# Optimization experiments

Hardware: AMD Instinct MI355X
Metric: run time of the kernel (lower is better)

The kernel has to match this reference:

```python
import jax, jax.numpy as jnp
import numpy as np

B, IN, OUT, GD, TD, H, W, L = 16, 512, 256, 256, 256, 32, 32, 32
EPS_BN = 1e-5


def _conv2d(x, w, pad):
    return jax.lax.conv_general_dilated(
        x, w, window_strides=(1, 1), padding=[(pad, pad), (pad, pad)],
        dimension_numbers=("NCHW", "OIHW", "NCHW"))


def _up2(x):
    return jnp.repeat(jnp.repeat(x, 2, axis=2), 2, axis=3)


def _l2n(v):  # F.normalize(p=2, dim=1), eps=1e-12
    n = jnp.sqrt(jnp.sum(v * v, axis=1, keepdims=True))
    return v / jnp.maximum(n, 1e-12)


def _context(img_embs, words_embs, mask):
    i = _l2n(img_embs)            # [B, TD, P]
    wd = _l2n(words_embs)         # [B, TD, L]
    sim = jnp.einsum("bcp,bcl->bpl", i, wd)
    sim = jnp.where(mask[:, None, :], -jnp.inf, sim)
    attn = jax.nn.softmax(sim, axis=-1)
    return jnp.einsum("bpl,bcl->bcp", attn, wd)  # [B, TD, P]


def _bn(x, w, b):  # training-mode BatchNorm2d, biased variance
    m = jnp.mean(x, axis=(0, 2, 3), keepdims=True)
    v = jnp.var(x, axis=(0, 2, 3), keepdims=True)
    return (x - m) * jax.lax.rsqrt(v + EPS_BN) * w[None, :, None, None] + b[None, :, None, None]


def setup_inputs():
    key = jax.random.key(0)
    ks = jax.random.split(key, 16)
    s = 0.02
    COND = GD + TD
    return {
        "x": jax.random.normal(ks[0], (B, IN, H, W), jnp.float32),
        "global_cond": jax.random.normal(ks[1], (B, GD), jnp.float32),
        "words_embs": jax.random.normal(ks[2], (B, TD, L), jnp.float32),
        "mask": jax.random.randint(ks[3], (B, L), 0, 2).astype(bool),
        "w_img1": jax.random.normal(ks[4], (TD, IN), jnp.float32) * s,
        "w_img2": jax.random.normal(ks[5], (TD, OUT), jnp.float32) * s,
        "w_c1": jax.random.normal(ks[6], (OUT, IN, 3, 3), jnp.float32) * s,
        "w_c2": jax.random.normal(ks[7], (OUT, OUT, 3, 3), jnp.float32) * s,
        "bn1_w": jnp.ones((IN,), jnp.float32),
        "bn1_b": jnp.zeros((IN,), jnp.float32),
        "bn2_w": jnp.ones((OUT,), jnp.float32),
        "bn2_b": jnp.zeros((OUT,), jnp.float32),
        "w_g1": jax.random.normal(ks[8], (IN, COND), jnp.float32) * s,
        "b_g1": jnp.zeros((IN,), jnp.float32),
        "w_b1": jax.random.normal(ks[9], (IN, COND), jnp.float32) * s,
        "b_b1": jnp.zeros((IN,), jnp.float32),
        "w_g2": jax.random.normal(ks[10], (OUT, COND), jnp.float32) * s,
        "b_g2": jnp.zeros((OUT,), jnp.float32),
        "w_b2": jax.random.normal(ks[11], (OUT, COND), jnp.float32) * s,
        "b_b2": jnp.zeros((OUT,), jnp.float32),
        "w_sc": jax.random.normal(ks[12], (OUT, IN, 1, 1), jnp.float32) * s,
        "b_sc": jnp.zeros((OUT,), jnp.float32),
    }


def reference(x, global_cond, words_embs, mask,
              w_img1, w_img2, w_c1, w_c2,
              bn1_w, bn1_b, bn2_w, bn2_b,
              w_g1, b_g1, w_b1, b_b1,
              w_g2, b_g2, w_b2, b_b2,
              w_sc, b_sc):
    # ---- residual path, stage 1 ----
    img1 = jnp.einsum("tc,bcp->btp", w_img1, x.reshape(B, IN, H * W))
    ctx1 = _context(img1, words_embs, mask)                 # [B, TD, H*W]
    gc = jnp.broadcast_to(global_cond[:, :, None], (B, GD, H * W))
    cond1 = jnp.concatenate([gc, ctx1], axis=1)             # [B, GD+TD, H*W]
    gamma1 = jnp.einsum("oc,bcp->bop", w_g1, cond1) + b_g1[None, :, None]
    beta1 = jnp.einsum("oc,bcp->bop", w_b1, cond1) + b_b1[None, :, None]
    out = gamma1.reshape(B, IN, H, W) * _bn(x, bn1_w, bn1_b) + beta1.reshape(B, IN, H, W)
    out = jax.nn.relu(out)
    out = _up2(out)                                         # [B, IN, 2H, 2W]
    out = _conv2d(out, w_c1, 1)                             # [B, OUT, 2H, 2W]
    h2, w2 = 2 * H, 2 * W
    # ---- residual path, stage 2 ----
    img2 = jnp.einsum("tc,bcp->btp", w_img2, out.reshape(B, OUT, h2 * w2))
    ctx2 = _context(img2, words_embs, mask)                 # [B, TD, h2*w2]
    gc2 = jnp.broadcast_to(global_cond[:, :, None], (B, GD, h2 * w2))
    cond2 = jnp.concatenate([gc2, ctx2], axis=1)
    gamma2 = jnp.einsum("oc,bcp->bop", w_g2, cond2) + b_g2[None, :, None]
    beta2 = jnp.einsum("oc,bcp->bop", w_b2, cond2) + b_b2[None, :, None]
    out = gamma2.reshape(B, OUT, h2, w2) * _bn(out, bn2_w, bn2_b) + beta2.reshape(B, OUT, h2, w2)
    out = jax.nn.relu(out)
    out = _conv2d(out, w_c2, 1)
    # ---- shortcut ----
    sc = _conv2d(_up2(x), w_sc, 0) + b_sc[None, :, None, None]
    return out + sc
```

## Files before the change

kernel.cpp:

```cpp
#include <hip/hip_runtime.h>
#include <hip/hip_bf16.h>
#include <math.h>

#define NB 16
#define CIN1 512
#define COUT 256
#define GD 256
#define TD 256
#define LL 32
#define P1 1024
#define P2 4096
#define CONDC 512

typedef __attribute__((ext_vector_type(8))) short bf16x8;
typedef __attribute__((ext_vector_type(4))) float f32x4;
typedef unsigned short u16;

__device__ __forceinline__ u16 f2b(float f) {
  __hip_bfloat16 h = __float2bfloat16(f);
  return *(u16*)&h;
}
__device__ __forceinline__ float b2f(u16 v) {
  unsigned u = ((unsigned)v) << 16;
  float f;
  __builtin_memcpy(&f, &u, 4);
  return f;
}

template <bool BF>
__global__ void bn_stats_kernel(const void* xv, float* __restrict__ mean,
                                float* __restrict__ rstd, int C, int HW) {
  int c = blockIdx.x, t = threadIdx.x;
  float s = 0.f, sq = 0.f;
  for (int b = 0; b < NB; ++b) {
    size_t base = ((size_t)b * C + c) * HW;
    for (int i = t; i < HW; i += 256) {
      float v = BF ? b2f(((const u16*)xv)[base + i]) : ((const float*)xv)[base + i];
      s += v; sq += v * v;
    }
  }
  __shared__ float ss[256], sq2[256];
  ss[t] = s; sq2[t] = sq; __syncthreads();
  for (int o = 128; o > 0; o >>= 1) {
    if (t < o) { ss[t] += ss[t + o]; sq2[t] += sq2[t + o]; }
    __syncthreads();
  }
  if (t == 0) {
    float n = (float)NB * (float)HW;
    float m = ss[0] / n;
    float v = sq2[0] / n - m * m;
    mean[c] = m;
    rstd[c] = rsqrtf(v + 1e-5f);
  }
}

__global__ void wdn_kernel(const float* __restrict__ we, float* __restrict__ wdn) {
  int b = blockIdx.x >> 5, l = blockIdx.x & 31;
  int t = threadIdx.x;
  const float* base = we + (size_t)b * TD * LL + l;
  float v[4]; float sq = 0.f;
#pragma unroll
  for (int k = 0; k < 4; ++k) { v[k] = base[(size_t)(t * 4 + k) * LL]; sq += v[k] * v[k]; }
#pragma unroll
  for (int o = 32; o > 0; o >>= 1) sq += __shfl_xor(sq, o);
  float r = 1.f / fmaxf(sqrtf(sq), 1e-12f);
  float* ob = wdn + (size_t)b * TD * LL + l;
#pragma unroll
  for (int k = 0; k < 4; ++k) ob[(size_t)(t * 4 + k) * LL] = v[k] * r;
}

__global__ void gvec_kernel(const float* __restrict__ Wg, const float* __restrict__ bias,
                            const float* __restrict__ gc, float* __restrict__ outv, int O) {
  int o = blockIdx.x * 64 + threadIdx.x;
  int b = blockIdx.y;
  if (o >= O) return;
  const float* wr = Wg + (size_t)o * CONDC;
  const float* g = gc + (size_t)b * GD;
  float s = 0.f;
  for (int c = 0; c < GD; ++c) s += wr[c] * g[c];
  outv[(size_t)b * O + o] = s + bias[o];
}

__global__ __launch_bounds__(256) void attnctx_kernel(
    const u16* __restrict__ img, const float* __restrict__ wdn,
    const int* __restrict__ mask, u16* __restrict__ ctx, int P) {
  __shared__ u16 imgT[64 * 72];
  __shared__ u16 wdnT[32 * 264];
  __shared__ u16 wdnC[256 * 40];
  __shared__ u16 attnB[64 * 40];
  __shared__ float sqP[4][64];
  __shared__ float rnL[64];
  const int b = blockIdx.y, p0 = blockIdx.x * 64;
  const int tid = threadIdx.x;
  const int w = tid >> 6, lane = tid & 63;
  const int l15 = lane & 15, lg = lane >> 4;
  const u16* ib = img + (size_t)b * TD * P;
  const float* wb = wdn + (size_t)b * TD * LL;

  for (int i = tid; i < TD * LL; i += 256) {
    int t = i >> 5, l = i & 31;
    u16 v = f2b(wb[i]);
    wdnT[l * 264 + t] = v;
    wdnC[t * 40 + l] = v;
  }

  f32x4 s0 = {}, s1 = {};
  float ssq = 0.f;
  for (int q = 0; q < 4; ++q) {
#pragma unroll
    for (int i = 0; i < 16; i += 2) {
      int t = q * 64 + w * 16 + i;
      u16 h0 = ib[(size_t)t * P + p0 + lane];
      u16 h1 = ib[(size_t)(t + 1) * P + p0 + lane];
      float v0 = b2f(h0), v1 = b2f(h1);
      ssq += v0 * v0 + v1 * v1;
      unsigned pk = (unsigned)h0 | ((unsigned)h1 << 16);
      *(unsigned*)(imgT + lane * 72 + w * 16 + i) = pk;
    }
    __syncthreads();
#pragma unroll
    for (int ks = 0; ks < 2; ++ks) {
      bf16x8 a = *(const bf16x8*)(imgT + (w * 16 + l15) * 72 + ks * 32 + lg * 8);
      bf16x8 b0 = *(const bf16x8*)(wdnT + l15 * 264 + q * 64 + ks * 32 + lg * 8);
      bf16x8 b1 = *(const bf16x8*)(wdnT + (16 + l15) * 264 + q * 64 + ks * 32 + lg * 8);
      s0 = __builtin_amdgcn_mfma_f32_16x16x32_bf16(a, b0, s0, 0, 0, 0);
      s1 = __builtin_amdgcn_mfma_f32_16x16x32_bf16(a, b1, s1, 0, 0, 0);
    }
    __syncthreads();
  }
  sqP[w][lane] = ssq;
  __syncthreads();
  if (tid < 64) {
    float s = sqP[0][tid] + sqP[1][tid] + sqP[2][tid] + sqP[3][tid];
    rnL[tid] = 1.f / fmaxf(sqrtf(s), 1e-12f);
  }
  __syncthreads();
  const bool m0 = mask[b * LL + l15] != 0;
  const bool m1 = mask[b * LL + 16 + l15] != 0;
#pragma unroll
  for (int k = 0; k < 4; ++k) {
    float rn = rnL[w * 16 + lg * 4 + k];
    float v0 = m0 ? -INFINITY : s0[k] * rn;
    float v1 = m1 ? -INFINITY : s1[k] * rn;
    float mx = fmaxf(v0, v1);
#pragma unroll
    for (int o = 1; o < 16; o <<= 1) mx = fmaxf(mx, __shfl_xor(mx, o));
    float e0 = expf(v0 - mx), e1 = expf(v1 - mx);
    float sm = e0 + e1;
#pragma unroll
    for (int o = 1; o < 16; o <<= 1) sm += __shfl_xor(sm, o);
    float inv = 1.f / sm;
    int px = w * 16 + lg * 4 + k;
    attnB[px * 40 + l15] = f2b(e0 * inv);
    attnB[px * 40 + 16 + l15] = f2b(e1 * inv);
  }
  __syncthreads();
  f32x4 acc[4][4] = {};
  bf16x8 bfr[4];
#pragma unroll
  for (int pt = 0; pt < 4; ++pt)
    bfr[pt] = *(const bf16x8*)(attnB + (pt * 16 + l15) * 40 + lg * 8);
#pragma unroll
  for (int cc = 0; cc < 4; ++cc) {
    bf16x8 a = *(const bf16x8*)(wdnC + ((w * 4 + cc) * 16 + l15) * 40 + lg * 8);
#pragma unroll
    for (int pt = 0; pt < 4; ++pt)
      acc[cc][pt] = __builtin_amdgcn_mfma_f32_16x16x32_bf16(a, bfr[pt], acc[cc][pt], 0, 0, 0);
  }
#pragma unroll
  for (int cc = 0; cc < 4; ++cc) {
#pragma unroll
    for (int pt = 0; pt < 4; ++pt) {
#pragma unroll
      for (int k = 0; k < 4; ++k) {
        int c = (w * 4 + cc) * 16 + lg * 4 + k;
        ctx[((size_t)b * TD + c) * P + p0 + pt * 16 + l15] = f2b(acc[cc][pt][k]);
      }
    }
  }
}

template <bool XB, bool YB>
__global__ __launch_bounds__(256, 2) void gemm_mfma_kernel(
    const float* __restrict__ W, int ldw, int c_off,
    const void* __restrict__ Xv, const float* __restrict__ vec,
    void* __restrict__ Yv, int T, int C, int P) {
  __shared__ u16 Wl[2][128 * 44];
  __shared__ u16 Xl[2][128 * 40];
  const int b = blockIdx.z;
  const int t0 = blockIdx.y * 128, p0 = blockIdx.x * 128;
  const int tid = threadIdx.x;
  const int w = tid >> 6, lane = tid & 63;
  const int wo = w >> 1, wq = w & 1;
  const int l15 = lane & 15, lg = lane >> 4;
  const int wr = tid >> 1, wcH = tid & 1;
  const int xr = tid >> 3, xcG = tid & 7;
  const int csw = xr ^ ((xcG & 3) << 3);
  const float* wsrc = W + (size_t)(t0 + wr) * ldw + c_off + wcH * 16;
  const float* xsrc32 = XB ? nullptr : (const float*)Xv + (size_t)b * C * P + (size_t)xr * P + p0 + xcG * 16;
  const u16* xsrc16 = XB ? (const u16*)Xv + (size_t)b * C * P + (size_t)xr * P + p0 + xcG * 16 : nullptr;
  const int NK = C / 32;
  f32x4 acc[4][4] = {};
  float4 wreg[4];
  u16 xst[16];

#pragma unroll
  for (int j = 0; j < 4; ++j) wreg[j] = *(const float4*)(wsrc + j * 4);
  if (XB) {
    union { u16 u[16]; uint4 q[2]; } xu;
    xu.q[0] = *(const uint4*)(xsrc16);
    xu.q[1] = *(const uint4*)(xsrc16 + 8);
#pragma unroll
    for (int i = 0; i < 16; ++i) xst[i] = xu.u[i];
  } else {
#pragma unroll
    for (int j = 0; j < 4; ++j) {
      float4 v = *(const float4*)(xsrc32 + j * 4);
      xst[j * 4 + 0] = f2b(v.x); xst[j * 4 + 1] = f2b(v.y);
      xst[j * 4 + 2] = f2b(v.z); xst[j * 4 + 3] = f2b(v.w);
    }
  }
  {
    u16* dst = Wl[0] + wr * 44 + wcH * 16;
#pragma unroll
    for (int j = 0; j < 4; ++j)
      *(ushort4*)(dst + j * 4) = make_ushort4(f2b(wreg[j].x), f2b(wreg[j].y), f2b(wreg[j].z), f2b(wreg[j].w));
#pragma unroll
    for (int i = 0; i < 16; ++i)
      Xl[0][(xcG * 16 + i) * 40 + csw] = xst[i];
  }
  __syncthreads();

  for (int kb = 0; kb < NK; ++kb) {
    const int cur = kb & 1;
    if (kb + 1 < NK) {
      const int c0n = (kb + 1) * 32;
#pragma unroll
      for (int j = 0; j < 4; ++j) wreg[j] = *(const float4*)(wsrc + c0n + j * 4);
      if (XB) {
        union { u16 u[16]; uint4 q[2]; } xu;
        xu.q[0] = *(const uint4*)(xsrc16 + (size_t)c0n * P);
        xu.q[1] = *(const uint4*)(xsrc16 + (size_t)c0n * P + 8);
#pragma unroll
        for (int i = 0; i < 16; ++i) xst[i] = xu.u[i];
      } else {
#pragma unroll
        for (int j = 0; j < 4; ++j) {
          float4 v = *(const float4*)(xsrc32 + (size_t)c0n * P + j * 4);
          xst[j * 4 + 0] = f2b(v.x); xst[j * 4 + 1] = f2b(v.y);
          xst[j * 4 + 2] = f2b(v.z); xst[j * 4 + 3] = f2b(v.w);
        }
      }
    }
    bf16x8 a[4], bb[4];
#pragma unroll
    for (int rr = 0; rr < 4; ++rr)
      a[rr] = *(const bf16x8*)(Wl[cur] + (wo * 64 + rr * 16 + l15) * 44 + lg * 8);
#pragma unroll
    for (int ss = 0; ss < 4; ++ss)
      bb[ss] = *(const bf16x8*)(Xl[cur] + (wq * 64 + ss * 16 + l15) * 40 + ((lg ^ ss) << 3));
#pragma unroll
    for (int rr = 0; rr < 4; ++rr)
#pragma unroll
      for (int ss = 0; ss < 4; ++ss)
        acc[rr][ss] = __builtin_amdgcn_mfma_f32_16x16x32_bf16(a[rr], bb[ss], acc[rr][ss], 0, 0, 0);
    if (kb + 1 < NK) {
      const int nxt = cur ^ 1;
      u16* dst = Wl[nxt] + wr * 44 + wcH * 16;
#pragma unroll
      for (int j = 0; j < 4; ++j)
        *(ushort4*)(dst + j * 4) = make_ushort4(f2b(wreg[j].x), f2b(wreg[j].y), f2b(wreg[j].z), f2b(wreg[j].w));
#pragma unroll
      for (int i = 0; i < 16; ++i)
        Xl[nxt][(xcG * 16 + i) * 40 + csw] = xst[i];
      __syncthreads();
    }
  }
#pragma unroll
  for (int rr = 0; rr < 4; ++rr) {
    int tb = t0 + wo * 64 + rr * 16 + lg * 4;
#pragma unroll
    for (int ss = 0; ss < 4; ++ss) {
      int p = p0 + wq * 64 + ss * 16 + l15;
#pragma unroll
      for (int k = 0; k < 4; ++k) {
        int t = tb + k;
        float val = acc[rr][ss][k];
        if (vec) val += vec[(size_t)b * T + t];
        if (YB) ((u16*)Yv)[((size_t)b * T + t) * P + p] = f2b(val);
        else    ((float*)Yv)[((size_t)b * T + t) * P + p] = val;
      }
    }
  }
}

template <bool XINB>
__global__ __launch_bounds__(256, 2) void gbact_kernel(
    const float* __restrict__ Wg, const float* __restrict__ Wb,
    const u16* __restrict__ ctx, const float* __restrict__ gvec,
    const float* __restrict__ bvec, const void* __restrict__ xinv,
    const float* __restrict__ mean, const float* __restrict__ rstd,
    const float* __restrict__ bnw, const float* __restrict__ bnb,
    u16* __restrict__ outb, int C, int P) {
  __shared__ u16 shmem[2][16384];
  const int b = blockIdx.z, t0 = blockIdx.y * 128, p0 = blockIdx.x * 128;
  const int tid = threadIdx.x;
  const int w = tid >> 6, lane = tid & 63;
  const int wo = w >> 1, wq = w & 1;
  const int l15 = lane & 15, lg = lane >> 4;
  const int wr = tid >> 1, wcH = tid & 1;
  const int xr = tid >> 3, xcG = tid & 7;
  const int csw = xr ^ ((xcG & 3) << 3);
  const float* gsrc = Wg + (size_t)(t0 + wr) * CONDC + GD + wcH * 16;
  const float* bsrc = Wb + (size_t)(t0 + wr) * CONDC + GD + wcH * 16;
  const u16* xsrc = ctx + (size_t)b * TD * P + (size_t)xr * P + p0 + xcG * 16;
  const int NK = TD / 32;
  f32x4 accg[4][4] = {}, accb[4][4] = {};
  float4 greg[4], breg[4];
  u16 xst[16];

#pragma unroll
  for (int j = 0; j < 4; ++j) {
    greg[j] = *(const float4*)(gsrc + j * 4);
    breg[j] = *(const float4*)(bsrc + j * 4);
  }
  {
    union { u16 u[16]; uint4 q[2]; } xu;
    xu.q[0] = *(const uint4*)(xsrc);
    xu.q[1] = *(const uint4*)(xsrc + 8);
#pragma unroll
    for (int i = 0; i < 16; ++i) xst[i] = xu.u[i];
  }
  {
    u16* dg = shmem[0] + wr * 44 + wcH * 16;
    u16* db = shmem[0] + 5632 + wr * 44 + wcH * 16;
    u16* xl = shmem[0] + 11264;
#pragma unroll
    for (int j = 0; j < 4; ++j) {
      *(ushort4*)(dg + j * 4) = make_ushort4(f2b(greg[j].x), f2b(greg[j].y), f2b(greg[j].z), f2b(greg[j].w));
      *(ushort4*)(db + j * 4) = make_ushort4(f2b(breg[j].x), f2b(breg[j].y), f2b(breg[j].z), f2b(breg[j].w));
    }
#pragma unroll
    for (int i = 0; i < 16; ++i)
      xl[(xcG * 16 + i) * 40 + csw] = xst[i];
  }
  __syncthreads();

  for (int kb = 0; kb < NK; ++kb) {
    const int cur = kb & 1;
    if (kb + 1 < NK) {
      const int c0n = (kb + 1) * 32;
#pragma unroll
      for (int j = 0; j < 4; ++j) {
        greg[j] = *(const float4*)(gsrc + c0n + j * 4);
        breg[j] = *(const float4*)(bsrc + c0n + j * 4);
      }
      union { u16 u[16]; uint4 q[2]; } xu;
      xu.q[0] = *(const uint4*)(xsrc + (size_t)c0n * P);
      xu.q[1] = *(const uint4*)(xsrc + (size_t)c0n * P + 8);
#pragma unroll
      for (int i = 0; i < 16; ++i) xst[i] = xu.u[i];
    }
    bf16x8 ag[4], ab[4], bb[4];
#pragma unroll
    for (int rr = 0; rr < 4; ++rr) {
      ag[rr] = *(const bf16x8*)(shmem[cur] + (wo * 64 + rr * 16 + l15) * 44 + lg * 8);
      ab[rr] = *(const bf16x8*)(shmem[cur] + 5632 + (wo * 64 + rr * 16 + l15) * 44 + lg * 8);
    }
#pragma unroll
    for (int ss = 0; ss < 4; ++ss)
      bb[ss] = *(const bf16x8*)(shmem[cur] + 11264 + (wq * 64 + ss * 16 + l15) * 40 + ((lg ^ ss) << 3));
#pragma unroll
    for (int rr = 0; rr < 4; ++rr)
#pragma unroll
      for (int ss = 0; ss < 4; ++ss) {
        accg[rr][ss] = __builtin_amdgcn_mfma_f32_16x16x32_bf16(ag[rr], bb[ss], accg[rr][ss], 0, 0, 0);
        accb[rr][ss] = __builtin_amdgcn_mfma_f32_16x16x32_bf16(ab[rr], bb[ss], accb[rr][ss], 0, 0, 0);
      }
    if (kb + 1 < NK) {
      const int nxt = cur ^ 1;
      u16* dg = shmem[nxt] + wr * 44 + wcH * 16;
      u16* db = shmem[nxt] + 5632 + wr * 44 + wcH * 16;
      u16* xl = shmem[nxt] + 11264;
#pragma unroll
      for (int j = 0; j < 4; ++j) {
        *(ushort4*)(dg + j * 4) = make_ushort4(f2b(greg[j].x), f2b(greg[j].y), f2b(greg[j].z), f2b(greg[j].w));
        *(ushort4*)(db + j * 4) = make_ushort4(f2b(breg[j].x), f2b(breg[j].y), f2b(breg[j].z), f2b(breg[j].w));
      }
#pragma unroll
      for (int i = 0; i < 16; ++i)
        xl[(xcG * 16 + i) * 40 + csw] = xst[i];
      __syncthreads();
    }
  }
  __syncthreads();
  u16* tbuf = &shmem[0][0];
#pragma unroll
  for (int rr = 0; rr < 4; ++rr) {
    float gv[4], bv[4], mm[4], rs[4], bB[4];
#pragma unroll
    for (int k = 0; k < 4; ++k) {
      int c = t0 + wo * 64 + rr * 16 + lg * 4 + k;
      gv[k] = gvec[(size_t)b * C + c];
      bv[k] = bvec[(size_t)b * C + c];
      mm[k] = mean[c]; rs[k] = rstd[c] * bnw[c]; bB[k] = bnb[c];
    }
#pragma unroll
    for (int ss = 0; ss < 4; ++ss) {
#pragma unroll
      for (int k = 0; k < 4; ++k) {
        int cl = wo * 64 + rr * 16 + lg * 4 + k;
        int pl = wq * 64 + ss * 16 + l15;
        size_t xidx = ((size_t)b * C + t0 + cl) * P + p0 + pl;
        float xv = XINB ? b2f(((const u16*)xinv)[xidx]) : ((const float*)xinv)[xidx];
        float g = accg[rr][ss][k] + gv[k];
        float be = accb[rr][ss][k] + bv[k];
        float val = fmaxf(g * ((xv - mm[k]) * rs[k] + bB[k]) + be, 0.f);
        tbuf[pl * 136 + cl] = f2b(val);
      }
    }
  }
  __syncthreads();
  const int pr = tid >> 1, h = tid & 1;
#pragma unroll
  for (int j = 0; j < 8; ++j) {
    uint4 v = *(uint4*)(tbuf + pr * 136 + h * 64 + j * 8);
    *(uint4*)(outb + ((size_t)b * P + p0 + pr) * C + t0 + h * 64 + j * 8) = v;
  }
}

__global__ void pack_w_kernel(const float* __restrict__ w, u16* __restrict__ wp, int O, int CIN) {
  int lin = blockIdx.x * 256 + threadIdx.x;
  if (lin >= O * CIN) return;
  int o = lin / CIN, c = lin - o * CIN;
  int c0blk = c >> 5, lg = (c >> 3) & 3, cc = c & 7;
  int ot = o >> 4, l15 = o & 15;
  int lane = lg * 16 + l15;
  size_t base = (((size_t)c0blk * (O >> 4) + ot) * 64 + lane) * 8 + cc;
  size_t posStride = (size_t)(CIN >> 5) * (O >> 4) * 512;
  const float* src = w + (size_t)lin * 9;
#pragma unroll
  for (int pos = 0; pos < 9; ++pos)
    wp[pos * posStride + base] = f2b(src[pos]);
}

template <int CIN, bool UP, bool OUTB>
__global__ __launch_bounds__(512, 2) void conv_mfma_kernel(
    const u16* __restrict__ Wp, const u16* __restrict__ Xt,
    const float* __restrict__ scs, const float* __restrict__ scb,
    void* __restrict__ Yv) {
  constexpr int S = UP ? 32 : 64;
  constexpr int NC0 = CIN >> 5;
  constexpr int NCH = 6 * 66 * 8;
  __shared__ u16 Xs[2][6 * 66 * 36];
  const int b = blockIdx.z, pxT = blockIdx.x;
  const int tid = threadIdx.x;
  const int w = tid >> 6, lane = tid & 63;
  const int wo = w >> 2, wp_ = w & 3;
  const int l15 = lane & 15, lg = lane >> 4;
  const int Y0 = pxT * 4;
  const u16* Xb = Xt + (size_t)b * S * S * CIN;
  const size_t posStride = (size_t)NC0 * 16 * 512;
  f32x4 acc[8][4] = {};
  uint2 st[7];

#pragma unroll
  for (int j = 0; j < 7; ++j) {
    int i = tid + j * 512;
    if (i < NCH) {
      int r = i / 528, rem = i - r * 528, col = rem >> 3, ch = rem & 7;
      int uy = Y0 - 1 + r, ux = col - 1;
      uint2 v = make_uint2(0u, 0u);
      if (uy >= 0 && uy < 64 && ux >= 0 && ux < 64) {
        int sy = UP ? (uy >> 1) : uy, sx = UP ? (ux >> 1) : ux;
        v = *(const uint2*)(Xb + ((size_t)sy * S + sx) * CIN + ch * 4);
      }
      st[j] = v;
    }
  }
#pragma unroll
  for (int j = 0; j < 7; ++j) {
    int i = tid + j * 512;
    if (i < NCH) {
      int r = i / 528, rem = i - r * 528, col = rem >> 3, ch = rem & 7;
      *(uint2*)(&Xs[0][(r * 66 + col) * 36 + ch * 4]) = st[j];
    }
  }
  __syncthreads();

  for (int c0b = 0; c0b < NC0; ++c0b) {
    const int cur = c0b & 1;
    if (c0b + 1 < NC0) {
      const int c0n = (c0b + 1) << 5;
#pragma unroll
      for (int j = 0; j < 7; ++j) {
        int i = tid + j * 512;
        if (i < NCH) {
          int r = i / 528, rem = i - r * 528, col = rem >> 3, ch = rem & 7;
          int uy = Y0 - 1 + r, ux = col - 1;
          uint2 v = make_uint2(0u, 0u);
          if (uy >= 0 && uy < 64 && ux >= 0 && ux < 64) {
            int sy = UP ? (uy >> 1) : uy, sx = UP ? (ux >> 1) : ux;
            v = *(const uint2*)(Xb + ((size_t)sy * S + sx) * CIN + c0n + ch * 4);
          }
          st[j] = v;
        }
      }
    }
    {
      const u16* wbB = Wp + ((size_t)c0b * 16 + wo * 8) * 512 + lane * 8;
      bf16x8 aC[8], aN[8];
#pragma unroll
      for (int rr = 0; rr < 8; ++rr)
        aC[rr] = *(const bf16x8*)(wbB + rr * 512);
#pragma unroll
      for (int pos = 0; pos < 9; ++pos) {
        const int ky = pos / 3, kx = pos - ky * 3;
        if (pos < 8) {
          const u16* wbn = wbB + (size_t)(pos + 1) * posStride;
#pragma unroll
          for (int rr = 0; rr < 8; ++rr)
            aN[rr] = *(const bf16x8*)(wbn + rr * 512);
        }
        const int rowb = ((wp_ + ky) * 66 + kx) * 36 + lg * 8;
#pragma unroll
        for (int ss = 0; ss < 4; ++ss) {
          int idx = rowb + (ss * 16 + l15) * 36;
          union { uint2 q[2]; bf16x8 v; } u;
          u.q[0] = *(const uint2*)(&Xs[cur][idx]);
          u.q[1] = *(const uint2*)(&Xs[cur][idx + 4]);
#pragma unroll
          for (int rr = 0; rr < 8; ++rr)
            acc[rr][ss] = __builtin_amdgcn_mfma_f32_16x16x32_bf16(aC[rr], u.v, acc[rr][ss], 0, 0, 0);
        }
#pragma unroll
        for (int rr = 0; rr < 8; ++rr) aC[rr] = aN[rr];
      }
    }
    if (c0b + 1 < NC0) {
#pragma unroll
      for (int j = 0; j < 7; ++j) {
        int i = tid + j * 512;
        if (i < NCH) {
          int r = i / 528, rem = i - r * 528, col = rem >> 3, ch = rem & 7;
          *(uint2*)(&Xs[cur ^ 1][(r * 66 + col) * 36 + ch * 4]) = st[j];
        }
      }
      __syncthreads();
    }
  }
  const int oBase = wo * 128 + lg * 4;
  const int pxBase = pxT * 256 + wp_ * 64 + l15;
  const int y = Y0 + wp_;
#pragma unroll
  for (int rr = 0; rr < 8; ++rr) {
#pragma unroll
    for (int ss = 0; ss < 4; ++ss) {
      int px = pxBase + ss * 16;
#pragma unroll
      for (int k = 0; k < 4; ++k) {
        int o = oBase + rr * 16 + k;
        float val = acc[rr][ss][k];
        if (scs) {
          int gx = px & 63;
          val += scs[((size_t)b * COUT + o) * P1 + (y >> 1) * 32 + (gx >> 1)] + scb[o];
        }
        if (OUTB) ((u16*)Yv)[((size_t)b * COUT + o) * 4096 + px] = f2b(val);
        else      ((float*)Yv)[((size_t)b * COUT + o) * 4096 + px] = val;
      }
    }
  }
}

extern "C" void kernel_launch(void* const* d_in, const int* in_sizes, int n_in,
                              void* d_out, int out_size, void* d_ws, size_t ws_size,
                              hipStream_t stream) {
  const float* x      = (const float*)d_in[0];
  const float* gcond  = (const float*)d_in[1];
  const float* wemb   = (const float*)d_in[2];
  const int*   mask   = (const int*)d_in[3];
  const float* w_img1 = (const float*)d_in[4];
  const float* w_img2 = (const float*)d_in[5];
  const float* w_c1   = (const float*)d_in[6];
  const float* w_c2   = (const float*)d_in[7];
  const float* bn1_w  = (const float*)d_in[8];
  const float* bn1_b  = (const float*)d_in[9];
  const float* bn2_w  = (const float*)d_in[10];
  const float* bn2_b  = (const float*)d_in[11];
  const float* w_g1   = (const float*)d_in[12];
  const float* b_g1   = (const float*)d_in[13];
  const float* w_b1   = (const float*)d_in[14];
  const float* b_b1   = (const float*)d_in[15];
  const float* w_g2   = (const float*)d_in[16];
  const float* b_g2   = (const float*)d_in[17];
  const float* w_b2   = (const float*)d_in[18];
  const float* b_b2   = (const float*)d_in[19];
  const float* w_sc   = (const float*)d_in[20];
  const float* b_sc   = (const float*)d_in[21];
  float* out = (float*)d_out;
  float* ws = (float*)d_ws;

  const size_t MF = 16777216;
  float* A  = ws;
  float* Br = ws + MF;
  float* Cr = ws + 2 * MF;
  float* SM = ws + 3 * MF;
  float* wdn   = SM;
  float* mean1 = SM + 131072;
  float* rstd1 = mean1 + 512;
  float* mean2 = rstd1 + 512;
  float* rstd2 = mean2 + 256;
  float* gvec1 = rstd2 + 256;
  float* bvec1 = gvec1 + 8192;
  float* gvec2 = bvec1 + 8192;
  float* bvec2 = gvec2 + 4096;
  float* wsp   = bvec2 + 4096;
  u16* Wp1 = (u16*)wsp;
  u16* Wp2 = (u16*)(wsp + 655360);

  u16* img1   = (u16*)A;
  u16* ctx1   = (u16*)A + 4194304;
  u16* Xt1    = (u16*)A + 8388608;
  u16* conv1o = (u16*)Cr;
  u16* img2   = (u16*)Br;
  u16* ctx2   = (u16*)A;
  u16* Xt2    = (u16*)Br;
  float* scs  = Cr;

  bn_stats_kernel<false><<<dim3(CIN1), dim3(256), 0, stream>>>(x, mean1, rstd1, CIN1, P1);
  wdn_kernel<<<dim3(NB * LL), dim3(64), 0, stream>>>(wemb, wdn);
  pack_w_kernel<<<dim3(COUT * CIN1 / 256), dim3(256), 0, stream>>>(w_c1, Wp1, COUT, CIN1);
  pack_w_kernel<<<dim3(COUT * COUT / 256), dim3(256), 0, stream>>>(w_c2, Wp2, COUT, COUT);
  gemm_mfma_kernel<false, true><<<dim3(P1 / 128, TD / 128, NB), dim3(256), 0, stream>>>(
      w_img1, CIN1, 0, x, nullptr, img1, TD, CIN1, P1);
  attnctx_kernel<<<dim3(P1 / 64, NB), dim3(256), 0, stream>>>(img1, wdn, mask, ctx1, P1);
  gvec_kernel<<<dim3(CIN1 / 64, NB), dim3(64), 0, stream>>>(w_g1, b_g1, gcond, gvec1, CIN1);
  gvec_kernel<<<dim3(CIN1 / 64, NB), dim3(64), 0, stream>>>(w_b1, b_b1, gcond, bvec1, CIN1);
  gbact_kernel<false><<<dim3(P1 / 128, CIN1 / 128, NB), dim3(256), 0, stream>>>(
      w_g1, w_b1, ctx1, gvec1, bvec1, x, mean1, rstd1, bn1_w, bn1_b, Xt1, CIN1, P1);
  conv_mfma_kernel<CIN1, true, true><<<dim3(16, 1, NB), dim3(512), 0, stream>>>(
      Wp1, Xt1, nullptr, nullptr, conv1o);

  bn_stats_kernel<true><<<dim3(COUT), dim3(256), 0, stream>>>(conv1o, mean2, rstd2, COUT, P2);
  gemm_mfma_kernel<true, true><<<dim3(P2 / 128, TD / 128, NB), dim3(256), 0, stream>>>(
      w_img2, COUT, 0, conv1o, nullptr, img2, TD, COUT, P2);
  attnctx_kernel<<<dim3(P2 / 64, NB), dim3(256), 0, stream>>>(img2, wdn, mask, ctx2, P2);
  gvec_kernel<<<dim3(COUT / 64, NB), dim3(64), 0, stream>>>(w_g2, b_g2, gcond, gvec2, COUT);
  gvec_kernel<<<dim3(COUT / 64, NB), dim3(64), 0, stream>>>(w_b2, b_b2, gcond, bvec2, COUT);
  gbact_kernel<true><<<dim3(P2 / 128, COUT / 128, NB), dim3(256), 0, stream>>>(
      w_g2, w_b2, ctx2, gvec2, bvec2, conv1o, mean2, rstd2, bn2_w, bn2_b, Xt2, COUT, P2);
  gemm_mfma_kernel<false, false><<<dim3(P1 / 128, COUT / 128, NB), dim3(256), 0, stream>>>(
      w_sc, CIN1, 0, x, nullptr, scs, COUT, CIN1, P1);
  conv_mfma_kernel<COUT, false, false><<<dim3(16, 1, NB), dim3(512), 0, stream>>>(
      Wp2, Xt2, scs, b_sc, out);
}
```

Baseline: 495.1 us.

## Fuse BN2 stats into conv1 epilogue, fold gvec into gbact, merge weight packs

Computes BatchNorm-2 per-channel sum and sum-of-squares in the conv1 epilogue: wave shuffles, LDS atomics, then per-block partials that a small finalize kernel reduces. This removes the separate bn_stats pass that reread conv1o. The global-cond projection (gvec) is now computed inside gbact per block, and the two weight-pack launches are merged into one. Together these drop five launches and one full activation read. In exchange each gbact block redoes a small 256-long dot product per row, and the stats are taken from fp32 accumulators rather than the bf16-rounded stored values.

```diff
diff --git a/kernel.cpp b/kernel.cpp
--- a/kernel.cpp
+++ b/kernel.cpp
@@ -54,6 +54,19 @@
   }
 }
 
+__global__ void bn_fin_kernel(const float* __restrict__ part, float* __restrict__ mean,
+                              float* __restrict__ rstd) {
+  int c = threadIdx.x;
+  float s = 0.f, sq = 0.f;
+  const float* ps = part + (size_t)c * 256;
+  const float* pq = part + 65536 + (size_t)c * 256;
+  for (int i = 0; i < 256; ++i) { s += ps[i]; sq += pq[i]; }
+  float n = 16.f * 4096.f;
+  float m = s / n;
+  mean[c] = m;
+  rstd[c] = rsqrtf(sq / n - m * m + 1e-5f);
+}
+
 __global__ void wdn_kernel(const float* __restrict__ we, float* __restrict__ wdn) {
   int b = blockIdx.x >> 5, l = blockIdx.x & 31;
   int t = threadIdx.x;
@@ -67,18 +80,6 @@
   float* ob = wdn + (size_t)b * TD * LL + l;
 #pragma unroll
   for (int k = 0; k < 4; ++k) ob[(size_t)(t * 4 + k) * LL] = v[k] * r;
-}
-
-__global__ void gvec_kernel(const float* __restrict__ Wg, const float* __restrict__ bias,
-                            const float* __restrict__ gc, float* __restrict__ outv, int O) {
-  int o = blockIdx.x * 64 + threadIdx.x;
-  int b = blockIdx.y;
-  if (o >= O) return;
-  const float* wr = Wg + (size_t)o * CONDC;
-  const float* g = gc + (size_t)b * GD;
-  float s = 0.f;
-  for (int c = 0; c < GD; ++c) s += wr[c] * g[c];
-  outv[(size_t)b * O + o] = s + bias[o];
 }
 
 __global__ __launch_bounds__(256) void attnctx_kernel(
@@ -296,13 +297,15 @@
 
 template <bool XINB>
 __global__ __launch_bounds__(256, 2) void gbact_kernel(
-    const float* __restrict__ Wg, const float* __restrict__ Wb,
-    const u16* __restrict__ ctx, const float* __restrict__ gvec,
-    const float* __restrict__ bvec, const void* __restrict__ xinv,
+    const float* __restrict__ Wg, const float* __restrict__ bg,
+    const float* __restrict__ Wb, const float* __restrict__ bb_,
+    const u16* __restrict__ ctx, const float* __restrict__ gcond,
+    const void* __restrict__ xinv,
     const float* __restrict__ mean, const float* __restrict__ rstd,
     const float* __restrict__ bnw, const float* __restrict__ bnb,
     u16* __restrict__ outb, int C, int P) {
   __shared__ u16 shmem[2][16384];
+  __shared__ float gvl[128], bvl[128];
   const int b = blockIdx.z, t0 = blockIdx.y * 128, p0 = blockIdx.x * 128;
   const int tid = threadIdx.x;
   const int w = tid >> 6, lane = tid & 63;
@@ -319,6 +322,20 @@
   float4 greg[4], breg[4];
   u16 xst[16];
 
+  {
+    int t = tid & 127;
+    const float* row = (tid < 128 ? Wg : Wb) + (size_t)(t0 + t) * CONDC;
+    const float* gc = gcond + (size_t)b * GD;
+    float s = 0.f;
+    for (int c = 0; c < GD; c += 4) {
+      float4 wv = *(const float4*)(row + c);
+      float4 gv4 = *(const float4*)(gc + c);
+      s += wv.x * gv4.x + wv.y * gv4.y + wv.z * gv4.z + wv.w * gv4.w;
+    }
+    s += (tid < 128 ? bg : bb_)[t0 + t];
+    if (tid < 128) gvl[t] = s; else bvl[t] = s;
+  }
+
 #pragma unroll
   for (int j = 0; j < 4; ++j) {
     greg[j] = *(const float4*)(gsrc + j * 4);
@@ -400,9 +417,10 @@
     float gv[4], bv[4], mm[4], rs[4], bB[4];
 #pragma unroll
     for (int k = 0; k < 4; ++k) {
-      int c = t0 + wo * 64 + rr * 16 + lg * 4 + k;
-      gv[k] = gvec[(size_t)b * C + c];
-      bv[k] = bvec[(size_t)b * C + c];
+      int cl = wo * 64 + rr * 16 + lg * 4 + k;
+      int c = t0 + cl;
+      gv[k] = gvl[cl];
+      bv[k] = bvl[cl];
       mm[k] = mean[c]; rs[k] = rstd[c] * bnw[c]; bB[k] = bnb[c];
     }
 #pragma unroll
@@ -429,30 +447,35 @@
   }
 }
 
-__global__ void pack_w_kernel(const float* __restrict__ w, u16* __restrict__ wp, int O, int CIN) {
+__global__ void pack2_kernel(const float* __restrict__ w1, u16* __restrict__ wp1,
+                             const float* __restrict__ w2, u16* __restrict__ wp2) {
   int lin = blockIdx.x * 256 + threadIdx.x;
-  if (lin >= O * CIN) return;
+  const int N1 = COUT * CIN1;
+  const float* w; u16* wp; int CIN;
+  if (lin < N1) { w = w1; wp = wp1; CIN = CIN1; }
+  else { lin -= N1; if (lin >= COUT * COUT) return; w = w2; wp = wp2; CIN = COUT; }
   int o = lin / CIN, c = lin - o * CIN;
   int c0blk = c >> 5, lg = (c >> 3) & 3, cc = c & 7;
   int ot = o >> 4, l15 = o & 15;
   int lane = lg * 16 + l15;
-  size_t base = (((size_t)c0blk * (O >> 4) + ot) * 64 + lane) * 8 + cc;
-  size_t posStride = (size_t)(CIN >> 5) * (O >> 4) * 512;
-  const float* src = w + (size_t)lin * 9;
+  size_t base = (((size_t)c0blk * (COUT >> 4) + ot) * 64 + lane) * 8 + cc;
+  size_t posStride = (size_t)(CIN >> 5) * (COUT >> 4) * 512;
+  const float* src = w + ((size_t)o * CIN + c) * 9;
 #pragma unroll
   for (int pos = 0; pos < 9; ++pos)
     wp[pos * posStride + base] = f2b(src[pos]);
 }
 
-template <int CIN, bool UP, bool OUTB>
+template <int CIN, bool UP, bool OUTB, bool STATS>
 __global__ __launch_bounds__(512, 2) void conv_mfma_kernel(
     const u16* __restrict__ Wp, const u16* __restrict__ Xt,
     const float* __restrict__ scs, const float* __restrict__ scb,
-    void* __restrict__ Yv) {
+    void* __restrict__ Yv, float* __restrict__ part) {
   constexpr int S = UP ? 32 : 64;
   constexpr int NC0 = CIN >> 5;
   constexpr int NCH = 6 * 66 * 8;
   __shared__ u16 Xs[2][6 * 66 * 36];
+  __shared__ float stats_ls[256], stats_lsq[256];
   const int b = blockIdx.z, pxT = blockIdx.x;
   const int tid = threadIdx.x;
   const int w = tid >> 6, lane = tid & 63;
@@ -463,6 +486,8 @@
   const size_t posStride = (size_t)NC0 * 16 * 512;
   f32x4 acc[8][4] = {};
   uint2 st[7];
+
+  if (STATS && tid < 256) { stats_ls[tid] = 0.f; stats_lsq[tid] = 0.f; }
 
 #pragma unroll
   for (int j = 0; j < 7; ++j) {
@@ -568,6 +593,30 @@
         if (OUTB) ((u16*)Yv)[((size_t)b * COUT + o) * 4096 + px] = f2b(val);
         else      ((float*)Yv)[((size_t)b * COUT + o) * 4096 + px] = val;
       }
+    }
+  }
+  if (STATS) {
+#pragma unroll
+    for (int rr = 0; rr < 8; ++rr) {
+#pragma unroll
+      for (int k = 0; k < 4; ++k) {
+        float s = acc[rr][0][k] + acc[rr][1][k] + acc[rr][2][k] + acc[rr][3][k];
+        float sq = acc[rr][0][k] * acc[rr][0][k] + acc[rr][1][k] * acc[rr][1][k] +
+                   acc[rr][2][k] * acc[rr][2][k] + acc[rr][3][k] * acc[rr][3][k];
+#pragma unroll
+        for (int o = 1; o < 16; o <<= 1) { s += __shfl_xor(s, o); sq += __shfl_xor(sq, o); }
+        if (l15 == 0) {
+          int o_ = oBase + rr * 16 + k;
+          atomicAdd(&stats_ls[o_], s);
+          atomicAdd(&stats_lsq[o_], sq);
+        }
+      }
+    }
+    __syncthreads();
+    if (tid < 256) {
+      int blk = b * 16 + pxT;
+      part[(size_t)tid * 256 + blk] = stats_ls[tid];
+      part[65536 + (size_t)tid * 256 + blk] = stats_lsq[tid];
     }
   }
 }
@@ -610,11 +659,8 @@
   float* rstd1 = mean1 + 512;
   float* mean2 = rstd1 + 512;
   float* rstd2 = mean2 + 256;
-  float* gvec1 = rstd2 + 256;
-  float* bvec1 = gvec1 + 8192;
-  float* gvec2 = bvec1 + 8192;
-  float* bvec2 = gvec2 + 4096;
-  float* wsp   = bvec2 + 4096;
+  float* part  = rstd2 + 256;
+  float* wsp   = part + 131072;
   u16* Wp1 = (u16*)wsp;
   u16* Wp2 = (u16*)(wsp + 655360);
 
@@ -629,28 +675,24 @@
 
   bn_stats_kernel<false><<<dim3(CIN1), dim3(256), 0, stream>>>(x, mean1, rstd1, CIN1, P1);
   wdn_kernel<<<dim3(NB * LL), dim3(64), 0, stream>>>(wemb, wdn);
-  pack_w_kernel<<<dim3(COUT * CIN1 / 256), dim3(256), 0, stream>>>(w_c1, Wp1, COUT, CIN1);
-  pack_w_kernel<<<dim3(COUT * COUT / 256), dim3(256), 0, stream>>>(w_c2, Wp2, COUT, COUT);
+  pack2_kernel<<<dim3((COUT * CIN1 + COUT * COUT) / 256), dim3(256), 0, stream>>>(
+      w_c1, Wp1, w_c2, Wp2);
   gemm_mfma_kernel<false, true><<<dim3(P1 / 128, TD / 128, NB), dim3(256), 0, stream>>>(
       w_img1, CIN1, 0, x, nullptr, img1, TD, CIN1, P1);
   attnctx_kernel<<<dim3(P1 / 64, NB), dim3(256), 0, stream>>>(img1, wdn, mask, ctx1, P1);
-  gvec_kernel<<<dim3(CIN1 / 64, NB), dim3(64), 0, stream>>>(w_g1, b_g1, gcond, gvec1, CIN1);
-  gvec_kernel<<<dim3(CIN1 / 64, NB), dim3(64), 0, stream>>>(w_b1, b_b1, gcond, bvec1, CIN1);
   gbact_kernel<false><<<dim3(P1 / 128, CIN1 / 128, NB), dim3(256), 0, stream>>>(
-      w_g1, w_b1, ctx1, gvec1, bvec1, x, mean1, rstd1, bn1_w, bn1_b, Xt1, CIN1, P1);
-  conv_mfma_kernel<CIN1, true, true><<<dim3(16, 1, NB), dim3(512), 0, stream>>>(
-      Wp1, Xt1, nullptr, nullptr, conv1o);
-
-  bn_stats_kernel<true><<<dim3(COUT), dim3(256), 0, stream>>>(conv1o, mean2, rstd2, COUT, P2);
+      w_g1, b_g1, w_b1, b_b1, ctx1, gcond, x, mean1, rstd1, bn1_w, bn1_b, Xt1, CIN1, P1);
+  conv_mfma_kernel<CIN1, true, true, true><<<dim3(16, 1, NB), dim3(512), 0, stream>>>(
+      Wp1, Xt1, nullptr, nullptr, conv1o, part);
+
+  bn_fin_kernel<<<dim3(1), dim3(256), 0, stream>>>(part, mean2, rstd2);
   gemm_mfma_kernel<true, true><<<dim3(P2 / 128, TD / 128, NB), dim3(256), 0, stream>>>(
       w_img2, COUT, 0, conv1o, nullptr, img2, TD, COUT, P2);
   attnctx_kernel<<<dim3(P2 / 64, NB), dim3(256), 0, stream>>>(img2, wdn, mask, ctx2, P2);
-  gvec_kernel<<<dim3(COUT / 64, NB), dim3(64), 0, stream>>>(w_g2, b_g2, gcond, gvec2, COUT);
-  gvec_kernel<<<dim3(COUT / 64, NB), dim3(64), 0, stream>>>(w_b2, b_b2, gcond, bvec2, COUT);
   gbact_kernel<true><<<dim3(P2 / 128, COUT / 128, NB), dim3(256), 0, stream>>>(
-      w_g2, w_b2, ctx2, gvec2, bvec2, conv1o, mean2, rstd2, bn2_w, bn2_b, Xt2, COUT, P2);
+      w_g2, b_g2, w_b2, b_b2, ctx2, gcond, conv1o, mean2, rstd2, bn2_w, bn2_b, Xt2, COUT, P2);
   gemm_mfma_kernel<false, false><<<dim3(P1 / 128, COUT / 128, NB), dim3(256), 0, stream>>>(
       w_sc, CIN1, 0, x, nullptr, scs, COUT, CIN1, P1);
-  conv_mfma_kernel<COUT, false, false><<<dim3(16, 1, NB), dim3(512), 0, stream>>>(
-      Wp2, Xt2, scs, b_sc, out);
-}
+  conv_mfma_kernel<COUT, false, false, false><<<dim3(16, 1, NB), dim3(512), 0, stream>>>(
+      Wp2, Xt2, scs, b_sc, out, nullptr);
+}
```

After: 470.0 us. 1.05x faster.
